# Optimization experiments

Hardware: AMD Instinct MI355X
Metric: run time of the kernel (lower is better)

The kernel has to match this reference:

```python
import jax, jax.numpy as jnp
import numpy as np

B, S, D = 8, 2048, 1024
G, V = 2, 320          # num_groups, codebook_size
DG = D // G            # 512, per-group codevector dim
DIVERSITY_WEIGHT = 0.1


def setup_inputs() -> dict:
    key = jax.random.key(0)
    k1, k2, k3, k4 = jax.random.split(key, 4)
    hidden_states = jax.random.normal(k1, (B, S, D), dtype=jnp.float32)
    W = jax.random.normal(k2, (G * V, D), dtype=jnp.float32)   # weight_proj weight (torch Linear layout)
    b = jax.random.normal(k3, (G * V,), dtype=jnp.float32)     # weight_proj bias
    codevectors = jax.random.normal(k4, (1, G * V, DG), dtype=jnp.float32)
    return {"hidden_states": hidden_states, "W": W, "b": b, "codevectors": codevectors}


def reference(hidden_states, W, b, codevectors):
    batch, seq, _ = hidden_states.shape
    n_tok = batch * seq
    # weight_proj: [B,S,D] -> [B,S,G*V]
    logits = jnp.einsum("bsd,vd->bsv", hidden_states, W) + b
    logits_flat = logits.reshape(n_tok * G, V)
    # eval path: hard argmax codevector selection
    codevector_idx = jnp.argmax(logits_flat, axis=-1)          # [n_tok*G]
    probs = jax.nn.one_hot(codevector_idx, V, dtype=logits.dtype)  # exact one-hot, [n_tok*G, V]
    probs_g = probs.reshape(n_tok, G, V)
    # perplexity over marginal code usage (mask_time_indices=None)
    marginal = probs_g.mean(axis=0)                            # [G, V]
    perplexity = jnp.exp(-jnp.sum(marginal * jnp.log(marginal + 1e-7), axis=-1)).sum()
    # codevector lookup: one-hot @ codebook == gather of row g*V + idx_g
    idx2 = codevector_idx.reshape(n_tok, G)                    # [n_tok, G]
    cb = codevectors.reshape(G * V, DG)
    rows = idx2 + jnp.arange(G, dtype=idx2.dtype) * V          # global codebook rows
    gathered = jnp.take(cb, rows, axis=0)                      # [n_tok, G, DG]
    out = gathered.reshape(batch, seq, G * DG)                 # [B, S, D]
    # faithful to original (buggy) reshape: view(batch, num_groups, seq)
    idx_out = codevector_idx.reshape(batch, G, seq)
    num_codevectors = G * V
    diversity_loss = (num_codevectors - perplexity) / num_codevectors * DIVERSITY_WEIGHT
    return out, idx_out, diversity_loss
```

## Files before the change

kernel.cpp:

```cpp
#include <hip/hip_runtime.h>
#include <hip/hip_bf16.h>
#include <math.h>
#include <stdint.h>

#define BATCH 8
#define SEQ   2048
#define DMODEL 1024
#define GROUPS 2
#define VOCAB 320
#define NOUT  (GROUPS*VOCAB)
#define DG    (DMODEL/GROUPS)
#define NTOK  (BATCH*SEQ)
#define NPAIR (NTOK*GROUPS)
#define NCHUNK 10

#define MARGIN 4.0f
#define NEG_INF (-3.0e38f)
#define MAXCAND 32

typedef __attribute__((ext_vector_type(8))) short short8;
typedef __attribute__((ext_vector_type(8))) unsigned short ushort8;
typedef __attribute__((ext_vector_type(4))) float f32x4;

__device__ __forceinline__ unsigned short f2bf(float f) {
    __hip_bfloat16 h = __float2bfloat16(f);
    return *reinterpret_cast<unsigned short*>(&h);
}
__device__ __forceinline__ float bf2f(unsigned short u) {
    unsigned int x = ((unsigned int)u) << 16;
    return __uint_as_float(x);
}

__device__ __forceinline__ void async16(const void* gptr, const void* lptr) {
    __builtin_amdgcn_global_load_lds(
        (const __attribute__((address_space(1))) unsigned int*)(unsigned long long)(uintptr_t)gptr,
        (__attribute__((address_space(3))) unsigned int*)(unsigned int)(uintptr_t)lptr,
        16, 0, 0);
}

#define NX4 (NTOK*DMODEL/4)
#define NW4 (NOUT*DMODEL/4)
__global__ __launch_bounds__(256) void convert_kernel(
    const float* __restrict__ X, const float* __restrict__ W,
    unsigned short* __restrict__ Xb, unsigned short* __restrict__ Wb)
{
    int i = blockIdx.x * 256 + threadIdx.x;
    const float4* src;
    ushort4* dst;
    int j;
    if (i < NX4) { src = (const float4*)X; dst = (ushort4*)Xb; j = i; }
    else         { src = (const float4*)W; dst = (ushort4*)Wb; j = i - NX4; if (j >= NW4) return; }
    float4 v = src[j];
    ushort4 u;
    u.x = f2bf(v.x); u.y = f2bf(v.y); u.z = f2bf(v.z); u.w = f2bf(v.w);
    dst[j] = u;
}

__global__ __launch_bounds__(256) void gemm_bf16_kernel(
    const unsigned short* __restrict__ Xb,
    const unsigned short* __restrict__ Wb,
    const float* __restrict__ bias,
    unsigned short* __restrict__ logits,
    float* __restrict__ rec_m1,
    float* __restrict__ rec_m2,
    int*   __restrict__ rec_id)
{
    __shared__ __align__(16) unsigned short As[128 * 32];
    __shared__ __align__(16) unsigned short Bs[128 * 32];

    const int tid  = threadIdx.x;
    const int lane = tid & 63;
    const int wave = tid >> 6;
    const int m0 = blockIdx.x * 128;
    const int n0 = blockIdx.y * 128;
    const int wm = (wave & 1) * 64;
    const int wn = (wave >> 1) * 64;

    f32x4 acc[4][4];
    #pragma unroll
    for (int a = 0; a < 4; a++)
        #pragma unroll
        for (int b = 0; b < 4; b++)
            acc[a][b] = (f32x4)0.0f;

    int aoff[2], boff[2], loff[2];
    #pragma unroll
    for (int j = 0; j < 2; j++) {
        int p = tid + j * 256;
        int r = p >> 2, s = p & 3;
        int c = s ^ ((r >> 1) & 3);
        aoff[j] = (m0 + r) * DMODEL + c * 8;
        boff[j] = (n0 + r) * DMODEL + c * 8;
        loff[j] = p * 8;
    }

    int afrag[4], bfrag[4];
    {
        int rho = lane & 15, h = lane >> 4;
        #pragma unroll
        for (int mi = 0; mi < 4; mi++) {
            int r = wm + mi * 16 + rho;
            afrag[mi] = (4 * r + (h ^ ((r >> 1) & 3))) * 8;
            int rn = wn + mi * 16 + rho;
            bfrag[mi] = (4 * rn + (h ^ ((rn >> 1) & 3))) * 8;
        }
    }

    for (int k0 = 0; k0 < DMODEL; k0 += 32) {
        #pragma unroll
        for (int j = 0; j < 2; j++) {
            async16(Xb + aoff[j] + k0, As + loff[j]);
            async16(Wb + boff[j] + k0, Bs + loff[j]);
        }
        __syncthreads();

        short8 af[4], bf[4];
        #pragma unroll
        for (int i = 0; i < 4; i++) {
            af[i] = *(const short8*)&As[afrag[i]];
            bf[i] = *(const short8*)&Bs[bfrag[i]];
        }
        #pragma unroll
        for (int mi = 0; mi < 4; mi++)
            #pragma unroll
            for (int ni = 0; ni < 4; ni++)
                acc[mi][ni] = __builtin_amdgcn_mfma_f32_16x16x32_bf16(
                    af[mi], bf[ni], acc[mi][ni], 0, 0, 0);
        __syncthreads();
    }

    const int colb = n0 + wn + (lane & 15);
    const int rowb = m0 + wm + (lane >> 4) * 4;
    const int chunk = (n0 + wn) >> 6;
    float bv[4];
    #pragma unroll
    for (int ni = 0; ni < 4; ni++) bv[ni] = bias[colb + ni * 16];

    #pragma unroll
    for (int mi = 0; mi < 4; mi++) {
        #pragma unroll
        for (int p = 0; p < 4; p++) {
            const int row = rowb + mi * 16 + p;
            float m1 = acc[mi][0][p] + bv[0];
            float m2 = NEG_INF;
            int i1 = colb;
            logits[row * NOUT + colb] = f2bf(m1);
            #pragma unroll
            for (int ni = 1; ni < 4; ni++) {
                float v = acc[mi][ni][p] + bv[ni];
                logits[row * NOUT + colb + ni * 16] = f2bf(v);
                if (v > m1) { m2 = m1; m1 = v; i1 = colb + ni * 16; }
                else        { m2 = fmaxf(m2, v); }
            }
            #pragma unroll
            for (int off = 1; off < 16; off <<= 1) {
                float om1 = __shfl_xor(m1, off);
                float om2 = __shfl_xor(m2, off);
                int   oi  = __shfl_xor(i1, off);
                float nm2 = fmaxf(fmaxf(m2, om2), fminf(m1, om1));
                if (om1 > m1 || (om1 == m1 && oi < i1)) { m1 = om1; i1 = oi; }
                m2 = nm2;
            }
            if ((lane & 15) == 0) {
                rec_m1[row * NCHUNK + chunk] = m1;
                rec_m2[row * NCHUNK + chunk] = m2;
                rec_id[row * NCHUNK + chunk] = i1;
            }
        }
    }
}

__global__ __launch_bounds__(256) void reduce_kernel(
    const float* __restrict__ rec_m1, const float* __restrict__ rec_m2,
    const int* __restrict__ rec_id,
    float* __restrict__ out_idx,
    unsigned long long* __restrict__ list, int* __restrict__ nAmb)
{
    const int pair = blockIdx.x * 256 + threadIdx.x;
    const int token = pair >> 1;
    const int g = pair & 1;
    const int base = token * NCHUNK + g * 5;

    float m1[5], m2s, M;
    int cstar = 0;
    #pragma unroll
    for (int c = 0; c < 5; c++) m1[c] = rec_m1[base + c];
    M = m1[0];
    #pragma unroll
    for (int c = 1; c < 5; c++)
        if (m1[c] > M) { M = m1[c]; cstar = c; }
    m2s = rec_m2[base + cstar];

    const float thr = M - MARGIN;
    bool amb = (m2s >= thr);
    #pragma unroll
    for (int c = 0; c < 5; c++)
        if (c != cstar && m1[c] >= thr) amb = true;

    if (!amb) {
        out_idx[pair] = (float)(rec_id[base + cstar] - g * VOCAB);
    } else {
        out_idx[pair] = -1.0f;
    }

    unsigned long long mask = __ballot(amb);
    if (mask) {
        const int lane = threadIdx.x & 63;
        const int leader = __ffsll((long long)mask) - 1;
        int basepos = 0;
        if (lane == leader) basepos = atomicAdd(nAmb, (int)__popcll(mask));
        basepos = __shfl(basepos, leader);
        if (amb) {
            int off = __popcll(mask & ((1ull << lane) - 1ull));
            list[basepos + off] =
                ((unsigned long long)__float_as_uint(M) << 32) | (unsigned int)pair;
        }
    }
}

__global__ __launch_bounds__(256) void extract_kernel(
    const unsigned short* __restrict__ logits,
    const unsigned long long* __restrict__ list, const int* __restrict__ nAmb,
    unsigned short* __restrict__ cand,
    int* __restrict__ cnt)
{
    const int wave = threadIdx.x >> 6;
    const int lane = threadIdx.x & 63;
    const int slot = blockIdx.x * 4 + wave;
    if (slot >= *nAmb) return;

    unsigned long long e = list[slot];
    const int pair = (int)(e & 0xFFFFFFFFull);
    const float M = __uint_as_float((unsigned int)(e >> 32));
    const int token = pair >> 1;
    const int g = pair & 1;

    const unsigned short* lp = logits + token * NOUT + g * VOCAB;
    const bool have = (lane < 40);
    float v[8];
    if (have) {
        ushort8 u = *(const ushort8*)(lp + lane * 8);
        #pragma unroll
        for (int j = 0; j < 8; j++) v[j] = bf2f(u[j]);
    } else {
        #pragma unroll
        for (int j = 0; j < 8; j++) v[j] = NEG_INF;
    }

    const float thr = M - MARGIN;
    unsigned short* cd = cand + (size_t)slot * MAXCAND;
    int total = 0;
    #pragma unroll
    for (int j = 0; j < 8; j++) {
        bool c = have && (v[j] >= thr);
        unsigned long long mask = __ballot(c);
        if (c) {
            int pos = total + __popcll(mask & ((1ull << lane) - 1ull));
            if (pos < MAXCAND) cd[pos] = (unsigned short)(lane * 8 + j);
        }
        total += (int)__popcll(mask);
    }
    if (lane == 0) cnt[slot] = (total < MAXCAND) ? total : MAXCAND;
}

__global__ __launch_bounds__(256) void rescore_kernel(
    const float* __restrict__ X, const float* __restrict__ W,
    const float* __restrict__ bias,
    const unsigned long long* __restrict__ list, const int* __restrict__ nAmb,
    const unsigned short* __restrict__ cand, const int* __restrict__ cnt,
    float* __restrict__ out_idx)
{
    const int lane  = threadIdx.x & 63;
    const int wglob = (blockIdx.x * 256 + threadIdx.x) >> 6;
    const int nwav  = gridDim.x * 4;
    const int n     = *nAmb;

    for (int slot = wglob; slot < n; slot += nwav) {
        const unsigned long long e = list[slot];
        const int pair  = (int)(e & 0xFFFFFFFFull);
        const int token = pair >> 1;
        const int g     = pair & 1;
        const int m     = cnt[slot];

        const float4* xr = (const float4*)(X + (size_t)token * DMODEL);
        float4 xv[4];
        #pragma unroll
        for (int q = 0; q < 4; q++) xv[q] = xr[lane + 64 * q];

        float best = NEG_INF;
        int bestcol = 0;
        for (int c = 0; c < m; c++) {
            const int col = (int)cand[(size_t)slot * MAXCAND + c];
            const float4* wr = (const float4*)(W + (size_t)(g * VOCAB + col) * DMODEL);
            float acc = 0.0f;
            #pragma unroll
            for (int q = 0; q < 4; q++) {
                float4 b = wr[lane + 64 * q];
                acc = fmaf(xv[q].x, b.x, acc);
                acc = fmaf(xv[q].y, b.y, acc);
                acc = fmaf(xv[q].z, b.z, acc);
                acc = fmaf(xv[q].w, b.w, acc);
            }
            #pragma unroll
            for (int off = 32; off >= 1; off >>= 1)
                acc += __shfl_xor(acc, off);
            const float logit = acc + bias[g * VOCAB + col];
            if (logit > best) { best = logit; bestcol = col; }
        }
        if (lane == 0) out_idx[pair] = (float)bestcol;
    }
}

__global__ __launch_bounds__(256) void gather_kernel(
    const float* __restrict__ cb,
    const float* __restrict__ out_idx,
    float* __restrict__ out,
    int* __restrict__ hist)
{
    __shared__ int gidx[32];
    const int t0 = blockIdx.x * 16;
    const int tid = threadIdx.x;

    if (tid < 32) {
        const int pair = t0 * 2 + tid;
        const int g = pair & 1;
        const int col = (int)out_idx[pair];
        gidx[tid] = g * VOCAB + col;
        atomicAdd(&hist[g * VOCAB + col], 1);
    }
    __syncthreads();

    const int g = tid >> 7;
    const int off4 = tid & 127;
    (void)g; (void)off4;
    #pragma unroll 4
    for (int i = 0; i < 16; i++) {
        const int token = t0 + i;
        const int gg = tid >> 7;
        const float4* src = (const float4*)(cb + (size_t)gidx[i * 2 + gg] * DG);
        ((float4*)(out + (size_t)token * DMODEL))[tid] = src[tid & 127];
    }
}

__global__ __launch_bounds__(256) void diversity_kernel(
    const int* __restrict__ hist, float* __restrict__ out_scalar)
{
    __shared__ float s0[256], s1[256];
    const int tid = threadIdx.x;
    float a0 = 0.0f, a1 = 0.0f;
    for (int i = tid; i < NOUT; i += 256) {
        float m = (float)hist[i] * (1.0f / (float)NTOK);
        float t = m * logf(m + 1e-7f);
        if (i < VOCAB) a0 += t; else a1 += t;
    }
    s0[tid] = a0; s1[tid] = a1;
    __syncthreads();
    for (int s = 128; s > 0; s >>= 1) {
        if (tid < s) { s0[tid] += s0[tid + s]; s1[tid] += s1[tid + s]; }
        __syncthreads();
    }
    if (tid == 0) {
        float perplexity = expf(-s0[0]) + expf(-s1[0]);
        *out_scalar = ((float)NOUT - perplexity) / (float)NOUT * 0.1f;
    }
}

extern "C" void kernel_launch(void* const* d_in, const int* in_sizes, int n_in,
                              void* d_out, int out_size, void* d_ws, size_t ws_size,
                              hipStream_t stream) {
    const float* X    = (const float*)d_in[0];
    const float* W    = (const float*)d_in[1];
    const float* bias = (const float*)d_in[2];
    const float* cb   = (const float*)d_in[3];

    float* out      = (float*)d_out;
    float* out_idx  = out + (size_t)NTOK * DMODEL;
    float* out_loss = out_idx + NPAIR;

    char* p = (char*)d_ws;
    unsigned short* Xb = (unsigned short*)p;      p += (size_t)NTOK * DMODEL * 2;
    unsigned short* Wb = (unsigned short*)p;      p += (size_t)NOUT * DMODEL * 2;
    unsigned short* logits = (unsigned short*)p;  p += (size_t)NTOK * NOUT * 2;
    float* rec_m1 = (float*)p;                    p += (size_t)NTOK * NCHUNK * 4;
    float* rec_m2 = (float*)p;                    p += (size_t)NTOK * NCHUNK * 4;
    int*   rec_id = (int*)p;                      p += (size_t)NTOK * NCHUNK * 4;
    unsigned long long* list = (unsigned long long*)p; p += (size_t)NPAIR * 8;
    unsigned short* cand = (unsigned short*)p;    p += (size_t)NPAIR * MAXCAND * 2;
    int* cnt = (int*)p;                           p += (size_t)NPAIR * 4;
    int* nAmb = (int*)p;                          p += 256;
    int* hist = (int*)p;                          p += NOUT * 4;

    size_t zbytes = 256 + NOUT * 4;
    hipMemsetAsync(nAmb, 0, zbytes, stream);

    convert_kernel<<<(NX4 + NW4) / 256, 256, 0, stream>>>(X, W, Xb, Wb);

    dim3 ggrid(NTOK / 128, NOUT / 128);
    gemm_bf16_kernel<<<ggrid, 256, 0, stream>>>(Xb, Wb, bias, logits,
                                                rec_m1, rec_m2, rec_id);

    reduce_kernel<<<NPAIR / 256, 256, 0, stream>>>(rec_m1, rec_m2, rec_id,
                                                   out_idx, list, nAmb);

    extract_kernel<<<NPAIR / 4, 256, 0, stream>>>(logits, list, nAmb, cand, cnt);

    rescore_kernel<<<2048, 256, 0, stream>>>(X, W, bias, list, nAmb,
                                             cand, cnt, out_idx);

    gather_kernel<<<NTOK / 16, 256, 0, stream>>>(cb, out_idx, out, hist);

    diversity_kernel<<<1, 256, 0, stream>>>(hist, out_loss);
}
```

Baseline: 209.1 us.

## Triple-buffer GEMM K-loop with async loads two stages ahead

Replaces the single-buffered shared-memory K loop, which stalled on every load, with a three-slot ring buffer. Loads for step t+2 are issued before computing step t, and a partial vmcnt wait plus a single barrier replace the two syncthreads per step. MFMA sections are also wrapped in s_setprio to favor the matrix work. The cost is three times the shared memory, which may reduce occupancy, and correctness now depends on the hand-written waitcnt counts matching the number of async loads each thread has in flight.

```diff
diff --git a/kernel.cpp b/kernel.cpp
--- a/kernel.cpp
+++ b/kernel.cpp
@@ -56,6 +56,7 @@
     dst[j] = u;
 }
 
+#define NKSTEP (DMODEL / 32)
 __global__ __launch_bounds__(256) void gemm_bf16_kernel(
     const unsigned short* __restrict__ Xb,
     const unsigned short* __restrict__ Wb,
@@ -65,8 +66,8 @@
     float* __restrict__ rec_m2,
     int*   __restrict__ rec_id)
 {
-    __shared__ __align__(16) unsigned short As[128 * 32];
-    __shared__ __align__(16) unsigned short Bs[128 * 32];
+    __shared__ __align__(16) unsigned short As[3][128 * 32];
+    __shared__ __align__(16) unsigned short Bs[3][128 * 32];
 
     const int tid  = threadIdx.x;
     const int lane = tid & 63;
@@ -106,28 +107,53 @@
         }
     }
 
-    for (int k0 = 0; k0 < DMODEL; k0 += 32) {
-        #pragma unroll
-        for (int j = 0; j < 2; j++) {
-            async16(Xb + aoff[j] + k0, As + loff[j]);
-            async16(Wb + boff[j] + k0, Bs + loff[j]);
-        }
-        __syncthreads();
-
-        short8 af[4], bf[4];
-        #pragma unroll
-        for (int i = 0; i < 4; i++) {
-            af[i] = *(const short8*)&As[afrag[i]];
-            bf[i] = *(const short8*)&Bs[bfrag[i]];
-        }
-        #pragma unroll
-        for (int mi = 0; mi < 4; mi++)
-            #pragma unroll
-            for (int ni = 0; ni < 4; ni++)
-                acc[mi][ni] = __builtin_amdgcn_mfma_f32_16x16x32_bf16(
-                    af[mi], bf[ni], acc[mi][ni], 0, 0, 0);
-        __syncthreads();
-    }
+    #define STAGE(T, BUF) do {                                          \
+        _Pragma("unroll")                                               \
+        for (int j = 0; j < 2; j++) {                                   \
+            async16(Xb + aoff[j] + (T) * 32, &As[BUF][loff[j]]);        \
+            async16(Wb + boff[j] + (T) * 32, &Bs[BUF][loff[j]]);        \
+        }                                                               \
+    } while (0)
+
+    #define COMPUTE(BUF) do {                                           \
+        short8 af_[4], bf_[4];                                          \
+        _Pragma("unroll")                                               \
+        for (int i = 0; i < 4; i++) {                                   \
+            af_[i] = *(const short8*)&As[BUF][afrag[i]];                \
+            bf_[i] = *(const short8*)&Bs[BUF][bfrag[i]];                \
+        }                                                               \
+        __builtin_amdgcn_s_setprio(1);                                  \
+        _Pragma("unroll")                                               \
+        for (int mi = 0; mi < 4; mi++)                                  \
+            _Pragma("unroll")                                           \
+            for (int ni = 0; ni < 4; ni++)                              \
+                acc[mi][ni] = __builtin_amdgcn_mfma_f32_16x16x32_bf16(  \
+                    af_[mi], bf_[ni], acc[mi][ni], 0, 0, 0);            \
+        __builtin_amdgcn_s_setprio(0);                                  \
+    } while (0)
+
+    STAGE(0, 0);
+    STAGE(1, 1);
+    asm volatile("s_waitcnt vmcnt(4)" ::: "memory");
+    __builtin_amdgcn_s_barrier();
+
+    int cb_ = 0;
+    for (int t = 0; t < NKSTEP - 2; ++t) {
+        int sb_ = cb_ + 2; if (sb_ >= 3) sb_ -= 3;
+        STAGE(t + 2, sb_);
+        COMPUTE(cb_);
+        asm volatile("s_waitcnt vmcnt(4)" ::: "memory");
+        __builtin_amdgcn_s_barrier();
+        cb_ = (cb_ == 2) ? 0 : cb_ + 1;
+    }
+    COMPUTE(cb_);
+    asm volatile("s_waitcnt vmcnt(0)" ::: "memory");
+    __builtin_amdgcn_s_barrier();
+    cb_ = (cb_ == 2) ? 0 : cb_ + 1;
+    COMPUTE(cb_);
+
+    #undef STAGE
+    #undef COMPUTE
 
     const int colb = n0 + wn + (lane & 15);
     const int rowb = m0 + wm + (lane >> 4) * 4;
@@ -330,9 +356,6 @@
     }
     __syncthreads();
 
-    const int g = tid >> 7;
-    const int off4 = tid & 127;
-    (void)g; (void)off4;
     #pragma unroll 4
     for (int i = 0; i < 16; i++) {
         const int token = t0 + i;
```

New measurement: 210.5 us. About the same (+0.7%).

## Shrink GEMM N-tile, fuse extract into rescore, fold memset and diversity into kernels

Applied to the files above, without the earlier changes.

The GEMM tile changes from 128x128 to 128x64, with each wave owning 32 rows across all 64 columns. This gives twice as many blocks, and the per-chunk max records now line up with the 64-column NCHUNK layout. The extract and rescore kernels merge into one resolve kernel that ballots candidates straight from the bf16 logits, removing the candidate buffer and its cap, and ties now go to the lower column. The memset moves into the convert kernel, and the diversity computation runs in the last block of the gather kernel behind an atomic counter, which cuts two launches. The costs are a smaller per-block compute tile with lower MFMA reuse, and a fence plus atomic at the end of the gather kernel.

```diff
diff --git a/kernel.cpp b/kernel.cpp
--- a/kernel.cpp
+++ b/kernel.cpp
@@ -16,7 +16,6 @@
 
 #define MARGIN 4.0f
 #define NEG_INF (-3.0e38f)
-#define MAXCAND 32
 
 typedef __attribute__((ext_vector_type(8))) short short8;
 typedef __attribute__((ext_vector_type(8))) unsigned short ushort8;
@@ -42,9 +41,14 @@
 #define NW4 (NOUT*DMODEL/4)
 __global__ __launch_bounds__(256) void convert_kernel(
     const float* __restrict__ X, const float* __restrict__ W,
-    unsigned short* __restrict__ Xb, unsigned short* __restrict__ Wb)
+    unsigned short* __restrict__ Xb, unsigned short* __restrict__ Wb,
+    int* __restrict__ nAmb, int* __restrict__ done, int* __restrict__ hist)
 {
     int i = blockIdx.x * 256 + threadIdx.x;
+    if (blockIdx.x == 0) {
+        for (int k = threadIdx.x; k < NOUT; k += 256) hist[k] = 0;
+        if (threadIdx.x == 0) { *nAmb = 0; *done = 0; }
+    }
     const float4* src;
     ushort4* dst;
     int j;
@@ -66,62 +70,67 @@
     int*   __restrict__ rec_id)
 {
     __shared__ __align__(16) unsigned short As[128 * 32];
-    __shared__ __align__(16) unsigned short Bs[128 * 32];
+    __shared__ __align__(16) unsigned short Bs[64 * 32];
 
     const int tid  = threadIdx.x;
     const int lane = tid & 63;
     const int wave = tid >> 6;
     const int m0 = blockIdx.x * 128;
-    const int n0 = blockIdx.y * 128;
-    const int wm = (wave & 1) * 64;
-    const int wn = (wave >> 1) * 64;
-
-    f32x4 acc[4][4];
-    #pragma unroll
-    for (int a = 0; a < 4; a++)
+    const int n0 = blockIdx.y * 64;
+    const int wm = wave * 32;
+
+    f32x4 acc[2][4];
+    #pragma unroll
+    for (int a = 0; a < 2; a++)
         #pragma unroll
         for (int b = 0; b < 4; b++)
             acc[a][b] = (f32x4)0.0f;
 
-    int aoff[2], boff[2], loff[2];
+    int aoff[2], loffA[2], boff, loffB;
     #pragma unroll
     for (int j = 0; j < 2; j++) {
         int p = tid + j * 256;
         int r = p >> 2, s = p & 3;
         int c = s ^ ((r >> 1) & 3);
         aoff[j] = (m0 + r) * DMODEL + c * 8;
-        boff[j] = (n0 + r) * DMODEL + c * 8;
-        loff[j] = p * 8;
-    }
-
-    int afrag[4], bfrag[4];
+        loffA[j] = p * 8;
+    }
+    {
+        int p = tid;
+        int r = p >> 2, s = p & 3;
+        int c = s ^ ((r >> 1) & 3);
+        boff = (n0 + r) * DMODEL + c * 8;
+        loffB = p * 8;
+    }
+
+    int afrag[2], bfrag[4];
     {
         int rho = lane & 15, h = lane >> 4;
         #pragma unroll
-        for (int mi = 0; mi < 4; mi++) {
+        for (int mi = 0; mi < 2; mi++) {
             int r = wm + mi * 16 + rho;
             afrag[mi] = (4 * r + (h ^ ((r >> 1) & 3))) * 8;
-            int rn = wn + mi * 16 + rho;
-            bfrag[mi] = (4 * rn + (h ^ ((rn >> 1) & 3))) * 8;
+        }
+        #pragma unroll
+        for (int ni = 0; ni < 4; ni++) {
+            int rn = ni * 16 + rho;
+            bfrag[ni] = (4 * rn + (h ^ ((rn >> 1) & 3))) * 8;
         }
     }
 
     for (int k0 = 0; k0 < DMODEL; k0 += 32) {
-        #pragma unroll
-        for (int j = 0; j < 2; j++) {
-            async16(Xb + aoff[j] + k0, As + loff[j]);
-            async16(Wb + boff[j] + k0, Bs + loff[j]);
-        }
+        async16(Xb + aoff[0] + k0, As + loffA[0]);
+        async16(Xb + aoff[1] + k0, As + loffA[1]);
+        async16(Wb + boff + k0, Bs + loffB);
         __syncthreads();
 
-        short8 af[4], bf[4];
-        #pragma unroll
-        for (int i = 0; i < 4; i++) {
-            af[i] = *(const short8*)&As[afrag[i]];
-            bf[i] = *(const short8*)&Bs[bfrag[i]];
-        }
-        #pragma unroll
-        for (int mi = 0; mi < 4; mi++)
+        short8 af[2], bf[4];
+        #pragma unroll
+        for (int mi = 0; mi < 2; mi++) af[mi] = *(const short8*)&As[afrag[mi]];
+        #pragma unroll
+        for (int ni = 0; ni < 4; ni++) bf[ni] = *(const short8*)&Bs[bfrag[ni]];
+        #pragma unroll
+        for (int mi = 0; mi < 2; mi++)
             #pragma unroll
             for (int ni = 0; ni < 4; ni++)
                 acc[mi][ni] = __builtin_amdgcn_mfma_f32_16x16x32_bf16(
@@ -129,15 +138,15 @@
         __syncthreads();
     }
 
-    const int colb = n0 + wn + (lane & 15);
+    const int colb = n0 + (lane & 15);
     const int rowb = m0 + wm + (lane >> 4) * 4;
-    const int chunk = (n0 + wn) >> 6;
+    const int chunk = blockIdx.y;
     float bv[4];
     #pragma unroll
     for (int ni = 0; ni < 4; ni++) bv[ni] = bias[colb + ni * 16];
 
     #pragma unroll
-    for (int mi = 0; mi < 4; mi++) {
+    for (int mi = 0; mi < 2; mi++) {
         #pragma unroll
         for (int p = 0; p < 4; p++) {
             const int row = rowb + mi * 16 + p;
@@ -218,56 +227,11 @@
     }
 }
 
-__global__ __launch_bounds__(256) void extract_kernel(
+__global__ __launch_bounds__(256) void resolve_kernel(
+    const float* __restrict__ X, const float* __restrict__ W,
+    const float* __restrict__ bias,
     const unsigned short* __restrict__ logits,
     const unsigned long long* __restrict__ list, const int* __restrict__ nAmb,
-    unsigned short* __restrict__ cand,
-    int* __restrict__ cnt)
-{
-    const int wave = threadIdx.x >> 6;
-    const int lane = threadIdx.x & 63;
-    const int slot = blockIdx.x * 4 + wave;
-    if (slot >= *nAmb) return;
-
-    unsigned long long e = list[slot];
-    const int pair = (int)(e & 0xFFFFFFFFull);
-    const float M = __uint_as_float((unsigned int)(e >> 32));
-    const int token = pair >> 1;
-    const int g = pair & 1;
-
-    const unsigned short* lp = logits + token * NOUT + g * VOCAB;
-    const bool have = (lane < 40);
-    float v[8];
-    if (have) {
-        ushort8 u = *(const ushort8*)(lp + lane * 8);
-        #pragma unroll
-        for (int j = 0; j < 8; j++) v[j] = bf2f(u[j]);
-    } else {
-        #pragma unroll
-        for (int j = 0; j < 8; j++) v[j] = NEG_INF;
-    }
-
-    const float thr = M - MARGIN;
-    unsigned short* cd = cand + (size_t)slot * MAXCAND;
-    int total = 0;
-    #pragma unroll
-    for (int j = 0; j < 8; j++) {
-        bool c = have && (v[j] >= thr);
-        unsigned long long mask = __ballot(c);
-        if (c) {
-            int pos = total + __popcll(mask & ((1ull << lane) - 1ull));
-            if (pos < MAXCAND) cd[pos] = (unsigned short)(lane * 8 + j);
-        }
-        total += (int)__popcll(mask);
-    }
-    if (lane == 0) cnt[slot] = (total < MAXCAND) ? total : MAXCAND;
-}
-
-__global__ __launch_bounds__(256) void rescore_kernel(
-    const float* __restrict__ X, const float* __restrict__ W,
-    const float* __restrict__ bias,
-    const unsigned long long* __restrict__ list, const int* __restrict__ nAmb,
-    const unsigned short* __restrict__ cand, const int* __restrict__ cnt,
     float* __restrict__ out_idx)
 {
     const int lane  = threadIdx.x & 63;
@@ -278,34 +242,50 @@
     for (int slot = wglob; slot < n; slot += nwav) {
         const unsigned long long e = list[slot];
         const int pair  = (int)(e & 0xFFFFFFFFull);
+        const float M   = __uint_as_float((unsigned int)(e >> 32));
         const int token = pair >> 1;
         const int g     = pair & 1;
-        const int m     = cnt[slot];
 
         const float4* xr = (const float4*)(X + (size_t)token * DMODEL);
         float4 xv[4];
         #pragma unroll
         for (int q = 0; q < 4; q++) xv[q] = xr[lane + 64 * q];
 
+        const unsigned short* lp = logits + token * NOUT + g * VOCAB;
+        const bool have = (lane < 40);
+        ushort8 u = (ushort8)0;
+        if (have) u = *(const ushort8*)(lp + lane * 8);
+
+        const float thr = M - MARGIN;
         float best = NEG_INF;
         int bestcol = 0;
-        for (int c = 0; c < m; c++) {
-            const int col = (int)cand[(size_t)slot * MAXCAND + c];
-            const float4* wr = (const float4*)(W + (size_t)(g * VOCAB + col) * DMODEL);
-            float acc = 0.0f;
-            #pragma unroll
-            for (int q = 0; q < 4; q++) {
-                float4 b = wr[lane + 64 * q];
-                acc = fmaf(xv[q].x, b.x, acc);
-                acc = fmaf(xv[q].y, b.y, acc);
-                acc = fmaf(xv[q].z, b.z, acc);
-                acc = fmaf(xv[q].w, b.w, acc);
+
+        #pragma unroll
+        for (int j = 0; j < 8; j++) {
+            bool c = have && (bf2f(u[j]) >= thr);
+            unsigned long long mask = __ballot(c);
+            while (mask) {
+                const int b = __ffsll((long long)mask) - 1;
+                mask &= mask - 1;
+                const int col = b * 8 + j;
+                const float4* wr = (const float4*)(W + (size_t)(g * VOCAB + col) * DMODEL);
+                float acc = 0.0f;
+                #pragma unroll
+                for (int q = 0; q < 4; q++) {
+                    float4 bb = wr[lane + 64 * q];
+                    acc = fmaf(xv[q].x, bb.x, acc);
+                    acc = fmaf(xv[q].y, bb.y, acc);
+                    acc = fmaf(xv[q].z, bb.z, acc);
+                    acc = fmaf(xv[q].w, bb.w, acc);
+                }
+                #pragma unroll
+                for (int off = 32; off >= 1; off >>= 1)
+                    acc += __shfl_xor(acc, off);
+                const float logit = acc + bias[g * VOCAB + col];
+                if (logit > best || (logit == best && col < bestcol)) {
+                    best = logit; bestcol = col;
+                }
             }
-            #pragma unroll
-            for (int off = 32; off >= 1; off >>= 1)
-                acc += __shfl_xor(acc, off);
-            const float logit = acc + bias[g * VOCAB + col];
-            if (logit > best) { best = logit; bestcol = col; }
         }
         if (lane == 0) out_idx[pair] = (float)bestcol;
     }
@@ -315,9 +295,12 @@
     const float* __restrict__ cb,
     const float* __restrict__ out_idx,
     float* __restrict__ out,
-    int* __restrict__ hist)
+    int* __restrict__ hist, int* __restrict__ done,
+    float* __restrict__ out_loss)
 {
     __shared__ int gidx[32];
+    __shared__ int lastFlag;
+    __shared__ float s0[256], s1[256];
     const int t0 = blockIdx.x * 16;
     const int tid = threadIdx.x;
 
@@ -330,9 +313,6 @@
     }
     __syncthreads();
 
-    const int g = tid >> 7;
-    const int off4 = tid & 127;
-    (void)g; (void)off4;
     #pragma unroll 4
     for (int i = 0; i < 16; i++) {
         const int token = t0 + i;
@@ -340,16 +320,16 @@
         const float4* src = (const float4*)(cb + (size_t)gidx[i * 2 + gg] * DG);
         ((float4*)(out + (size_t)token * DMODEL))[tid] = src[tid & 127];
     }
-}
-
-__global__ __launch_bounds__(256) void diversity_kernel(
-    const int* __restrict__ hist, float* __restrict__ out_scalar)
-{
-    __shared__ float s0[256], s1[256];
-    const int tid = threadIdx.x;
+
+    __threadfence();
+    if (tid == 0) lastFlag = (atomicAdd(done, 1) == (int)gridDim.x - 1);
+    __syncthreads();
+    if (!lastFlag) return;
+
     float a0 = 0.0f, a1 = 0.0f;
     for (int i = tid; i < NOUT; i += 256) {
-        float m = (float)hist[i] * (1.0f / (float)NTOK);
+        int h = atomicAdd(&hist[i], 0);
+        float m = (float)h * (1.0f / (float)NTOK);
         float t = m * logf(m + 1e-7f);
         if (i < VOCAB) a0 += t; else a1 += t;
     }
@@ -361,7 +341,7 @@
     }
     if (tid == 0) {
         float perplexity = expf(-s0[0]) + expf(-s1[0]);
-        *out_scalar = ((float)NOUT - perplexity) / (float)NOUT * 0.1f;
+        *out_loss = ((float)NOUT - perplexity) / (float)NOUT * 0.1f;
     }
 }
 
@@ -385,29 +365,23 @@
     float* rec_m2 = (float*)p;                    p += (size_t)NTOK * NCHUNK * 4;
     int*   rec_id = (int*)p;                      p += (size_t)NTOK * NCHUNK * 4;
     unsigned long long* list = (unsigned long long*)p; p += (size_t)NPAIR * 8;
-    unsigned short* cand = (unsigned short*)p;    p += (size_t)NPAIR * MAXCAND * 2;
-    int* cnt = (int*)p;                           p += (size_t)NPAIR * 4;
     int* nAmb = (int*)p;                          p += 256;
+    int* done = (int*)p;                          p += 256;
     int* hist = (int*)p;                          p += NOUT * 4;
 
-    size_t zbytes = 256 + NOUT * 4;
-    hipMemsetAsync(nAmb, 0, zbytes, stream);
-
-    convert_kernel<<<(NX4 + NW4) / 256, 256, 0, stream>>>(X, W, Xb, Wb);
-
-    dim3 ggrid(NTOK / 128, NOUT / 128);
+    convert_kernel<<<(NX4 + NW4) / 256, 256, 0, stream>>>(X, W, Xb, Wb,
+                                                          nAmb, done, hist);
+
+    dim3 ggrid(NTOK / 128, NOUT / 64);
     gemm_bf16_kernel<<<ggrid, 256, 0, stream>>>(Xb, Wb, bias, logits,
                                                 rec_m1, rec_m2, rec_id);
 
     reduce_kernel<<<NPAIR / 256, 256, 0, stream>>>(rec_m1, rec_m2, rec_id,
                                                    out_idx, list, nAmb);
 
-    extract_kernel<<<NPAIR / 4, 256, 0, stream>>>(logits, list, nAmb, cand, cnt);
-
-    rescore_kernel<<<2048, 256, 0, stream>>>(X, W, bias, list, nAmb,
-                                             cand, cnt, out_idx);
-
-    gather_kernel<<<NTOK / 16, 256, 0, stream>>>(cb, out_idx, out, hist);
-
-    diversity_kernel<<<1, 256, 0, stream>>>(hist, out_loss);
-}
+    resolve_kernel<<<2048, 256, 0, stream>>>(X, W, bias, logits, list, nAmb,
+                                             out_idx);
+
+    gather_kernel<<<NTOK / 16, 256, 0, stream>>>(cb, out_idx, out,
+                                                 hist, done, out_loss);
+}
```

Result: slower. 336.3 us (+60.8%).
